# Kernel tuning notes

Hardware: AMD Instinct MI355X
Metric: run time of the kernel (lower is better)

The kernel has to match this reference:

```python
import jax, jax.numpy as jnp
import numpy as np

B, N, MW, H, C, K = 64, 8192, 128, 8, 1024, 3
HD = C // H  # head width = 128


def setup_inputs() -> dict:
    key = jax.random.key(0)
    ks = jax.random.split(key, 16)
    s = 0.02
    return {
        "control_state": jax.random.normal(ks[0], (B, C), jnp.float32),
        "memory": jax.random.normal(ks[1], (B, N, MW), jnp.float32),
        "prev_weights": jax.nn.softmax(jax.random.normal(ks[2], (B, H, N), jnp.float32), axis=-1),
        "defaults": jax.nn.softmax(jax.random.normal(ks[3], (B, H, N), jnp.float32), axis=-1),
        "W_head": s * jax.random.normal(ks[4], (C, H * HD), jnp.float32),
        "b_head": jnp.zeros((H, HD), jnp.float32),
        "W_reset": s * jax.random.normal(ks[5], (H, HD, 1), jnp.float32),
        "b_reset": jnp.zeros((H, 1), jnp.float32),
        "W_key": s * jax.random.normal(ks[6], (H, HD, MW), jnp.float32),
        "b_key": jnp.zeros((H, MW), jnp.float32),
        "W_beta": s * jax.random.normal(ks[7], (H, HD, 1), jnp.float32),
        "b_beta": jnp.zeros((H, 1), jnp.float32),
        "W_gate": s * jax.random.normal(ks[8], (H, HD, 1), jnp.float32),
        "b_gate": jnp.zeros((H, 1), jnp.float32),
        "W_shift": s * jax.random.normal(ks[9], (H, HD, K), jnp.float32),
        "b_shift": jnp.zeros((H, K), jnp.float32),
        "W_gamma": s * jax.random.normal(ks[10], (H, HD, 1), jnp.float32),
        "b_gamma": jnp.zeros((H, 1), jnp.float32),
        "merge_w": jax.random.normal(ks[11], (H,), jnp.float32) * 0.3 + 1.0 / H,
    }


def reference(control_state, memory, prev_weights, defaults, W_head, b_head,
              W_reset, b_reset, W_key, b_key, W_beta, b_beta, W_gate, b_gate,
              W_shift, b_shift, W_gamma, b_gamma, merge_w):
    eps = 1e-8
    # head projection: [B,C] -> [B,H,HD]
    heads = (control_state @ W_head).reshape(-1, H, HD) + b_head
    # sigmoid reset gate: convex blend of prior weights with defaults
    reset_p = jax.nn.sigmoid(jnp.einsum('bhd,hdo->bho', heads, W_reset) + b_reset)  # [B,H,1]
    weights = prev_weights * (1.0 - reset_p) + defaults * reset_p
    # NTM addressing parameters (per-head linear maps)
    key_ = jnp.einsum('bhd,hdw->bhw', heads, W_key) + b_key          # [B,H,MW]
    beta = jax.nn.softplus(jnp.einsum('bhd,hdo->bho', heads, W_beta) + b_beta)   # [B,H,1]
    gate = jax.nn.sigmoid(jnp.einsum('bhd,hdo->bho', heads, W_gate) + b_gate)    # [B,H,1]
    shift = jax.nn.softmax(jnp.einsum('bhd,hdk->bhk', heads, W_shift) + b_shift, axis=-1)  # [B,H,K]
    gamma = 1.0 + jax.nn.softplus(jnp.einsum('bhd,hdo->bho', heads, W_gamma) + b_gamma)    # [B,H,1]
    # content addressing: sharpened cosine similarity softmax over memory slots
    sim = jnp.einsum('bhw,bnw->bhn', key_, memory)
    sim = sim / (jnp.linalg.norm(key_, axis=-1, keepdims=True)
                 * jnp.linalg.norm(memory, axis=-1)[:, None, :] + eps)
    content = jax.nn.softmax(beta * sim, axis=-1)                    # [B,H,N]
    # interpolate with (possibly reset) prior weights
    w_g = gate * content + (1.0 - gate) * weights
    # location addressing: circular convolution with shift kernel symmetric around 0
    w_s = sum(shift[..., j:j + 1] * jnp.roll(w_g, j - K // 2, axis=-1) for j in range(K))
    # sharpening
    w_pow = (w_s + eps) ** gamma
    new_w = w_pow / jnp.sum(w_pow, axis=-1, keepdims=True)           # [B,H,N]
    # read: per-head attention matmul against memory, then weighted head merge
    headed = jnp.einsum('bhn,bnw->bhw', new_w, memory)               # [B,H,MW]
    out = jnp.einsum('bhw,h->bw', headed, merge_w)                   # [B,MW]
    return out, new_w
```

## Files before the change

kernel.cpp:

```cpp
#include <hip/hip_runtime.h>
#include <hip/hip_bf16.h>
#include <math.h>

#define Bb 64
#define Nn 8192
#define MWw 128
#define Hh 8
#define Cc 1024
#define HDd 128
#define Kk 3

__device__ __forceinline__ float dot4(float4 a, float4 b) {
  return a.x*b.x + a.y*b.y + a.z*b.z + a.w*b.w;
}
__device__ __forceinline__ float sigmoidf_(float x) { return 1.0f / (1.0f + __expf(-x)); }
__device__ __forceinline__ float softplusf_(float x) {
  return fmaxf(x, 0.0f) + log1pf(__expf(-fabsf(x)));
}

__global__ __launch_bounds__(1024) void k_params(
    const float* __restrict__ cs, const float* __restrict__ W_head, const float* __restrict__ b_head,
    const float* __restrict__ W_reset, const float* __restrict__ b_reset,
    const float* __restrict__ W_key, const float* __restrict__ b_key,
    const float* __restrict__ W_beta, const float* __restrict__ b_beta,
    const float* __restrict__ W_gate, const float* __restrict__ b_gate,
    const float* __restrict__ W_shift, const float* __restrict__ b_shift,
    const float* __restrict__ W_gamma, const float* __restrict__ b_gamma,
    float* __restrict__ key_ws, float* __restrict__ params,
    float* __restrict__ zs, float* __restrict__ outp)
{
  int bh = blockIdx.x;
  int b = bh >> 3, h = bh & 7;
  int t = threadIdx.x;
  int d = t & 127, sl = t >> 7;
  __shared__ float red[8][128];
  __shared__ float head_s[128];
  __shared__ float key_s[128];
  __shared__ float wred[16];

  if (bh == 0) {
    zs[t] = 0.0f;
    #pragma unroll
    for (int j = 0; j < 8; ++j) outp[j * 1024 + t] = 0.0f;
  }

  const float* csb = cs + b * Cc + sl * 128;
  const float* w0 = W_head + (size_t)(sl * 128) * (Hh * HDd) + h * HDd + d;
  float acc = 0.0f;
  #pragma unroll 8
  for (int c = 0; c < 128; ++c) acc = fmaf(csb[c], w0[(size_t)c * (Hh * HDd)], acc);
  red[sl][d] = acc;
  __syncthreads();
  if (t < 128) {
    float s = b_head[h * HDd + t];
    #pragma unroll
    for (int j = 0; j < 8; ++j) s += red[j][t];
    head_s[t] = s;
  }
  __syncthreads();

  {
    const float* wk = W_key + (size_t)h * HDd * MWw + (sl * 16) * MWw + d;
    float ka = 0.0f;
    #pragma unroll
    for (int dd = 0; dd < 16; ++dd) ka = fmaf(head_s[sl * 16 + dd], wk[dd * MWw], ka);
    red[sl][d] = ka;
  }
  __syncthreads();
  if (t < 128) {
    float kv = b_key[h * MWw + t];
    #pragma unroll
    for (int j = 0; j < 8; ++j) kv += red[j][t];
    key_ws[bh * MWw + t] = kv;
    key_s[t] = kv;
  }
  __syncthreads();

  float hd = head_s[d];
  float v;
  switch (sl) {
    case 0: v = hd * W_reset[h * HDd + d]; break;
    case 1: v = hd * W_beta[h * HDd + d]; break;
    case 2: v = hd * W_gate[h * HDd + d]; break;
    case 3: v = hd * W_gamma[h * HDd + d]; break;
    case 4: v = hd * W_shift[(h * HDd + d) * Kk + 0]; break;
    case 5: v = hd * W_shift[(h * HDd + d) * Kk + 1]; break;
    case 6: v = hd * W_shift[(h * HDd + d) * Kk + 2]; break;
    default: v = key_s[d] * key_s[d]; break;
  }
  v += __shfl_xor(v, 1, 64);
  v += __shfl_xor(v, 2, 64);
  v += __shfl_xor(v, 4, 64);
  v += __shfl_xor(v, 8, 64);
  v += __shfl_xor(v, 16, 64);
  v += __shfl_xor(v, 32, 64);
  if ((t & 63) == 0) wred[t >> 6] = v;
  __syncthreads();
  if (t == 0) {
    float r0 = wred[0]  + wred[1];
    float r1 = wred[2]  + wred[3];
    float r2 = wred[4]  + wred[5];
    float r3 = wred[6]  + wred[7];
    float r4 = wred[8]  + wred[9];
    float r5 = wred[10] + wred[11];
    float r6 = wred[12] + wred[13];
    float r7 = wred[14] + wred[15];
    float reset = sigmoidf_(r0 + b_reset[h]);
    float beta  = softplusf_(r1 + b_beta[h]);
    float gate  = sigmoidf_(r2 + b_gate[h]);
    float gamma = 1.0f + softplusf_(r3 + b_gamma[h]);
    float a0 = r4 + b_shift[h * Kk + 0];
    float a1 = r5 + b_shift[h * Kk + 1];
    float a2 = r6 + b_shift[h * Kk + 2];
    float mx = fmaxf(a0, fmaxf(a1, a2));
    float e0 = __expf(a0 - mx), e1 = __expf(a1 - mx), e2 = __expf(a2 - mx);
    float inv = 1.0f / (e0 + e1 + e2);
    float* P = params + bh * 8;
    P[0] = reset; P[1] = beta; P[2] = gate; P[3] = gamma;
    P[4] = e0 * inv; P[5] = e1 * inv; P[6] = e2 * inv;
    P[7] = sqrtf(r7);
  }
}

__global__ __launch_bounds__(256, 2) void k_sim(
    const float* __restrict__ mem, const float* __restrict__ key_ws,
    const float* __restrict__ params, float* __restrict__ e_ws, float* __restrict__ Z)
{
  int b = blockIdx.y, chunk = blockIdx.x;
  int t = threadIdx.x;
  int lane = t & 63, wid = t >> 6;
  int sub = lane & 7, rid = lane >> 3;
  __shared__ float4 keys[8][32];
  __shared__ float betas[8], knorms[8];
  __shared__ float e_s[8][520];
  if (t < 8) { betas[t] = params[(b * 8 + t) * 8 + 1]; knorms[t] = params[(b * 8 + t) * 8 + 7]; }
  {
    int h = t >> 5, q = t & 31;
    keys[h][q] = ((const float4*)key_ws)[(b * 8 + h) * 32 + q];
  }
  __syncthreads();

  float4 kreg[8][4];
  #pragma unroll
  for (int h2 = 0; h2 < 8; ++h2) {
    kreg[h2][0] = keys[h2][sub];
    kreg[h2][1] = keys[h2][sub + 8];
    kreg[h2][2] = keys[h2][sub + 16];
    kreg[h2][3] = keys[h2][sub + 24];
  }

  const float4* m4 = (const float4*)mem + (size_t)b * Nn * 32;
  float beta = betas[sub], kn = knorms[sub];
  float zloc = 0.0f;
  int n0 = chunk * 512;

  #pragma unroll 1
  for (int itr = 0; itr < 8; ++itr) {
    int nb = n0 + itr * 64 + wid * 16 + rid;
    float4 m[2][4];
    float nrm[2];
    float acc[2][8];
    #pragma unroll
    for (int r = 0; r < 2; ++r) {
      const float4* rp = m4 + (size_t)(nb + r * 8) * 32 + sub;
      m[r][0] = rp[0]; m[r][1] = rp[8]; m[r][2] = rp[16]; m[r][3] = rp[24];
    }
    #pragma unroll
    for (int r = 0; r < 2; ++r) {
      nrm[r] = dot4(m[r][0], m[r][0]) + dot4(m[r][1], m[r][1])
             + dot4(m[r][2], m[r][2]) + dot4(m[r][3], m[r][3]);
      #pragma unroll
      for (int h2 = 0; h2 < 8; ++h2) {
        acc[r][h2] = dot4(m[r][0], kreg[h2][0]) + dot4(m[r][1], kreg[h2][1])
                   + dot4(m[r][2], kreg[h2][2]) + dot4(m[r][3], kreg[h2][3]);
      }
    }
    #pragma unroll
    for (int r = 0; r < 2; ++r) {
      float* a = acc[r];
      bool h1 = (sub & 1) != 0;
      float v40 = (h1 ? a[1] : a[0]) + __shfl_xor(h1 ? a[0] : a[1], 1, 64);
      float v41 = (h1 ? a[3] : a[2]) + __shfl_xor(h1 ? a[2] : a[3], 1, 64);
      float v42 = (h1 ? a[5] : a[4]) + __shfl_xor(h1 ? a[4] : a[5], 1, 64);
      float v43 = (h1 ? a[7] : a[6]) + __shfl_xor(h1 ? a[6] : a[7], 1, 64);
      bool h2b = (sub & 2) != 0;
      float v20 = (h2b ? v41 : v40) + __shfl_xor(h2b ? v40 : v41, 2, 64);
      float v21 = (h2b ? v43 : v42) + __shfl_xor(h2b ? v42 : v43, 2, 64);
      bool h4 = (sub & 4) != 0;
      float dsum = (h4 ? v21 : v20) + __shfl_xor(h4 ? v20 : v21, 4, 64);
      float nr = nrm[r];
      nr += __shfl_xor(nr, 1, 64);
      nr += __shfl_xor(nr, 2, 64);
      nr += __shfl_xor(nr, 4, 64);
      float s = beta * dsum / (kn * sqrtf(nr) + 1e-8f);
      float e = __expf(s - beta);
      e_s[sub][(nb + r * 8) - n0] = e;
      zloc += e;
    }
  }
  zloc += __shfl_xor(zloc, 8, 64);
  zloc += __shfl_xor(zloc, 16, 64);
  zloc += __shfl_xor(zloc, 32, 64);
  if (lane < 8) atomicAdd(&Z[b * 8 + lane], zloc);
  __syncthreads();

  #pragma unroll
  for (int j = 0; j < 4; ++j) {
    int idx = j * 256 + t;
    int h = idx >> 7, q = idx & 127;
    float4 v = *(const float4*)&e_s[h][q * 4];
    ((float4*)(e_ws + (size_t)(b * 8 + h) * Nn + n0))[q] = v;
  }
}

__global__ __launch_bounds__(256) void k_conv(
    const float* __restrict__ e_ws, const float* __restrict__ prev, const float* __restrict__ defw,
    const float* __restrict__ params, const float* __restrict__ Z,
    float* __restrict__ wp, float* __restrict__ S)
{
  int chunk = blockIdx.x, h = blockIdx.y, b = blockIdx.z;
  int bh = b * 8 + h, t = threadIdx.x;
  __shared__ float wg[2052];
  const float* P = params + bh * 8;
  float reset = P[0], gate = P[2], gamma = P[3], s0 = P[4], s1 = P[5], s2 = P[6];
  float invZg = gate / Z[bh];
  float om = 1.0f - gate, omr = 1.0f - reset;
  size_t base = (size_t)bh * Nn;
  int n0 = chunk * 2048;

  const float4* e4p = (const float4*)(e_ws + base + n0);
  const float4* p4p = (const float4*)(prev + base + n0);
  const float4* d4p = (const float4*)(defw + base + n0);
  #pragma unroll
  for (int it = 0; it < 2; ++it) {
    int idx4 = it * 256 + t;
    float4 e = e4p[idx4], pv = p4p[idx4], dv = d4p[idx4];
    float4 w;
    w.x = invZg * e.x + om * (pv.x * omr + dv.x * reset);
    w.y = invZg * e.y + om * (pv.y * omr + dv.y * reset);
    w.z = invZg * e.z + om * (pv.z * omr + dv.z * reset);
    w.w = invZg * e.w + om * (pv.w * omr + dv.w * reset);
    *(float4*)&wg[idx4 * 4] = w;
  }
  if (t < 2) {
    int n = (t == 0) ? ((n0 + Nn - 1) & (Nn - 1)) : ((n0 + 2048) & (Nn - 1));
    float e = e_ws[base + n], pv = prev[base + n], dv = defw[base + n];
    wg[2048 + t] = invZg * e + om * (pv * omr + dv * reset);
  }
  __syncthreads();

  float sacc = 0.0f;
  float4* wp4 = (float4*)(wp + base + n0);
  #pragma unroll
  for (int it = 0; it < 2; ++it) {
    int idx4 = it * 256 + t;
    int l = idx4 * 4;
    float4 c = *(const float4*)&wg[l];
    float left  = (l == 0)        ? wg[2048] : wg[l - 1];
    float right = (l + 4 == 2048) ? wg[2049] : wg[l + 4];
    float4 wsv;
    wsv.x = s0 * c.y   + s1 * c.x + s2 * left;
    wsv.y = s0 * c.z   + s1 * c.y + s2 * c.x;
    wsv.z = s0 * c.w   + s1 * c.z + s2 * c.y;
    wsv.w = s0 * right + s1 * c.w + s2 * c.z;
    float4 o;
    o.x = __expf(gamma * __logf(wsv.x + 1e-8f));
    o.y = __expf(gamma * __logf(wsv.y + 1e-8f));
    o.z = __expf(gamma * __logf(wsv.z + 1e-8f));
    o.w = __expf(gamma * __logf(wsv.w + 1e-8f));
    wp4[idx4] = o;
    sacc += o.x + o.y + o.z + o.w;
  }
  sacc += __shfl_xor(sacc, 1, 64);
  sacc += __shfl_xor(sacc, 2, 64);
  sacc += __shfl_xor(sacc, 4, 64);
  sacc += __shfl_xor(sacc, 8, 64);
  sacc += __shfl_xor(sacc, 16, 64);
  sacc += __shfl_xor(sacc, 32, 64);
  __shared__ float sred[4];
  if ((t & 63) == 0) sred[t >> 6] = sacc;
  __syncthreads();
  if (t == 0) atomicAdd(&S[bh], sred[0] + sred[1] + sred[2] + sred[3]);
}

__global__ __launch_bounds__(256) void k_readnorm(
    const float* __restrict__ mem, float* __restrict__ wp, const float* __restrict__ S,
    const float* __restrict__ merge_w, float* __restrict__ out)
{
  int b = blockIdx.y; int n0 = blockIdx.x * 512; int t = threadIdx.x;
  __shared__ float kh[8], invS_s[8];
  __shared__ float coef_s[512];
  __shared__ float4 red4[256];
  if (t < 8) {
    float s = S[b * 8 + t];
    invS_s[t] = 1.0f / s;
    kh[t] = merge_w[t] / s;
  }
  __syncthreads();

  int col = t & 127, grp = t >> 7;
  float4 cf = make_float4(0.0f, 0.0f, 0.0f, 0.0f);
  #pragma unroll
  for (int hh = 0; hh < 4; ++hh) {
    int h = grp * 4 + hh;
    float4* wph = (float4*)(wp + (size_t)(b * 8 + h) * Nn + n0);
    float4 v = wph[col];
    float is = invS_s[h], k = kh[h];
    float4 o;
    o.x = v.x * is; o.y = v.y * is; o.z = v.z * is; o.w = v.w * is;
    wph[col] = o;
    cf.x = fmaf(k, v.x, cf.x);
    cf.y = fmaf(k, v.y, cf.y);
    cf.z = fmaf(k, v.z, cf.z);
    cf.w = fmaf(k, v.w, cf.w);
  }
  red4[grp * 128 + col] = cf;
  __syncthreads();
  if (t < 128) {
    float4 a = red4[t], c = red4[128 + t];
    float4 s4;
    s4.x = a.x + c.x; s4.y = a.y + c.y; s4.z = a.z + c.z; s4.w = a.w + c.w;
    *(float4*)&coef_s[t * 4] = s4;
  }
  __syncthreads();

  int w4 = t & 31, rg = t >> 5;
  const float4* m4 = (const float4*)mem + (size_t)b * Nn * 32;
  float4 acc = make_float4(0.0f, 0.0f, 0.0f, 0.0f);
  #pragma unroll 4
  for (int it = 0; it < 64; ++it) {
    int nl = it * 8 + rg;
    float c = coef_s[nl];
    float4 m = m4[(size_t)(n0 + nl) * 32 + w4];
    acc.x = fmaf(c, m.x, acc.x);
    acc.y = fmaf(c, m.y, acc.y);
    acc.z = fmaf(c, m.z, acc.z);
    acc.w = fmaf(c, m.w, acc.w);
  }
  red4[t] = acc;
  __syncthreads();
  if (t < 32) {
    float4 s = red4[t];
    #pragma unroll
    for (int j = 1; j < 8; ++j) {
      float4 o = red4[t + 32 * j];
      s.x += o.x; s.y += o.y; s.z += o.z; s.w += o.w;
    }
    atomicAdd(&out[b * MWw + t * 4 + 0], s.x);
    atomicAdd(&out[b * MWw + t * 4 + 1], s.y);
    atomicAdd(&out[b * MWw + t * 4 + 2], s.z);
    atomicAdd(&out[b * MWw + t * 4 + 3], s.w);
  }
}

extern "C" void kernel_launch(void* const* d_in, const int* in_sizes, int n_in,
                              void* d_out, int out_size, void* d_ws, size_t ws_size,
                              hipStream_t stream)
{
  const float* cs      = (const float*)d_in[0];
  const float* mem     = (const float*)d_in[1];
  const float* prev    = (const float*)d_in[2];
  const float* defw    = (const float*)d_in[3];
  const float* W_head  = (const float*)d_in[4];
  const float* b_head  = (const float*)d_in[5];
  const float* W_reset = (const float*)d_in[6];
  const float* b_reset = (const float*)d_in[7];
  const float* W_key   = (const float*)d_in[8];
  const float* b_key   = (const float*)d_in[9];
  const float* W_beta  = (const float*)d_in[10];
  const float* b_beta  = (const float*)d_in[11];
  const float* W_gate  = (const float*)d_in[12];
  const float* b_gate  = (const float*)d_in[13];
  const float* W_shift = (const float*)d_in[14];
  const float* b_shift = (const float*)d_in[15];
  const float* W_gamma = (const float*)d_in[16];
  const float* b_gamma = (const float*)d_in[17];
  const float* merge_w = (const float*)d_in[18];

  float* out  = (float*)d_out;
  float* neww = out + Bb * MWw;

  float* ws_f   = (float*)d_ws;
  float* key_ws = ws_f;
  float* params = ws_f + 65536;
  float* Zacc   = ws_f + 69632;
  float* Sacc   = ws_f + 70144;
  float* e_ws   = ws_f + 70656;

  k_params<<<dim3(Bb * Hh), dim3(1024), 0, stream>>>(
      cs, W_head, b_head, W_reset, b_reset, W_key, b_key, W_beta, b_beta,
      W_gate, b_gate, W_shift, b_shift, W_gamma, b_gamma, key_ws, params,
      Zacc, out);
  k_sim<<<dim3(16, Bb), dim3(256), 0, stream>>>(mem, key_ws, params, e_ws, Zacc);
  k_conv<<<dim3(4, Hh, Bb), dim3(256), 0, stream>>>(e_ws, prev, defw, params, Zacc, neww, Sacc);
  k_readnorm<<<dim3(16, Bb), dim3(256), 0, stream>>>(mem, neww, Sacc, merge_w, out);
}
```

Measured before the change: 495.1 us.

## Fuse similarity, convolution and read stages into one grid-synchronised kernel

```diff
diff --git a/kernel.cpp b/kernel.cpp
--- a/kernel.cpp
+++ b/kernel.cpp
@@ -1,5 +1,4 @@
 #include <hip/hip_runtime.h>
-#include <hip/hip_bf16.h>
 #include <math.h>
 
 #define Bb 64
@@ -16,6 +15,21 @@
 __device__ __forceinline__ float sigmoidf_(float x) { return 1.0f / (1.0f + __expf(-x)); }
 __device__ __forceinline__ float softplusf_(float x) {
   return fmaxf(x, 0.0f) + log1pf(__expf(-fabsf(x)));
+}
+
+__device__ __forceinline__ void grid_barrier(unsigned* bar, unsigned target) {
+  __syncthreads();
+  if (threadIdx.x == 0) {
+    __threadfence();
+    __hip_atomic_fetch_add(bar, 1u, __ATOMIC_ACQ_REL, __HIP_MEMORY_SCOPE_AGENT);
+    int spins = 0;
+    while (__hip_atomic_load(bar, __ATOMIC_ACQUIRE, __HIP_MEMORY_SCOPE_AGENT) < target) {
+      __builtin_amdgcn_s_sleep(8);
+      if (++spins > (1 << 22)) break;
+    }
+    __threadfence();
+  }
+  __syncthreads();
 }
 
 __global__ __launch_bounds__(1024) void k_params(
@@ -40,6 +54,7 @@
 
   if (bh == 0) {
     zs[t] = 0.0f;
+    if (t < 16) zs[1024 + t] = 0.0f;
     #pragma unroll
     for (int j = 0; j < 8; ++j) outp[j * 1024 + t] = 0.0f;
   }
@@ -122,22 +137,34 @@
   }
 }
 
-__global__ __launch_bounds__(256, 2) void k_sim(
+#define ESTRIDE 1032
+
+__global__ __launch_bounds__(256, 2) void k_fused(
     const float* __restrict__ mem, const float* __restrict__ key_ws,
-    const float* __restrict__ params, float* __restrict__ e_ws, float* __restrict__ Z)
+    const float* __restrict__ params, const float* __restrict__ prev,
+    const float* __restrict__ defw, const float* __restrict__ merge_w,
+    float* __restrict__ Z, float* __restrict__ S, float* __restrict__ eh,
+    unsigned* __restrict__ bar, float* __restrict__ neww, float* __restrict__ out)
 {
-  int b = blockIdx.y, chunk = blockIdx.x;
+  int c = blockIdx.x, b = blockIdx.y;
   int t = threadIdx.x;
   int lane = t & 63, wid = t >> 6;
   int sub = lane & 7, rid = lane >> 3;
+  int n0 = c * 1024;
+
   __shared__ float4 keys[8][32];
   __shared__ float betas[8], knorms[8];
-  __shared__ float e_s[8][520];
+  __shared__ float e_s[8 * ESTRIDE];
+  __shared__ float pL[64];
+  __shared__ float zL[8];
+  __shared__ float wgh[2][8];
+  __shared__ float kh_s[8], invS_s[8];
+  __shared__ float coef_s[1024];
+  __shared__ float4 red4[256];
+
   if (t < 8) { betas[t] = params[(b * 8 + t) * 8 + 1]; knorms[t] = params[(b * 8 + t) * 8 + 7]; }
-  {
-    int h = t >> 5, q = t & 31;
-    keys[h][q] = ((const float4*)key_ws)[(b * 8 + h) * 32 + q];
-  }
+  { int h = t >> 5, q = t & 31;
+    keys[h][q] = ((const float4*)key_ws)[(b * 8 + h) * 32 + q]; }
   __syncthreads();
 
   float4 kreg[8][4];
@@ -152,17 +179,16 @@
   const float4* m4 = (const float4*)mem + (size_t)b * Nn * 32;
   float beta = betas[sub], kn = knorms[sub];
   float zloc = 0.0f;
-  int n0 = chunk * 512;
 
   #pragma unroll 1
-  for (int itr = 0; itr < 8; ++itr) {
-    int nb = n0 + itr * 64 + wid * 16 + rid;
+  for (int itr = 0; itr < 16; ++itr) {
+    int nl = itr * 64 + wid * 16 + rid;
     float4 m[2][4];
     float nrm[2];
     float acc[2][8];
     #pragma unroll
     for (int r = 0; r < 2; ++r) {
-      const float4* rp = m4 + (size_t)(nb + r * 8) * 32 + sub;
+      const float4* rp = m4 + (size_t)(n0 + nl + r * 8) * 32 + sub;
       m[r][0] = rp[0]; m[r][1] = rp[8]; m[r][2] = rp[16]; m[r][3] = rp[24];
     }
     #pragma unroll
@@ -194,7 +220,7 @@
       nr += __shfl_xor(nr, 4, 64);
       float s = beta * dsum / (kn * sqrtf(nr) + 1e-8f);
       float e = __expf(s - beta);
-      e_s[sub][(nb + r * 8) - n0] = e;
+      e_s[sub * ESTRIDE + nl + r * 8] = e;
       zloc += e;
     }
   }
@@ -203,148 +229,137 @@
   zloc += __shfl_xor(zloc, 32, 64);
   if (lane < 8) atomicAdd(&Z[b * 8 + lane], zloc);
   __syncthreads();
+  if (t < 16) {
+    int hh = t & 7, side = t >> 3;
+    __hip_atomic_store(&eh[(b * 8 + c) * 16 + side * 8 + hh],
+                       e_s[hh * ESTRIDE + (side ? 1023 : 0)],
+                       __ATOMIC_RELAXED, __HIP_MEMORY_SCOPE_AGENT);
+  }
+  grid_barrier(&bar[0], 512u);
+
+  if (t < 64) pL[t] = params[b * 64 + t];
+  if (t < 8)
+    zL[t] = __hip_atomic_load(&Z[b * 8 + t], __ATOMIC_RELAXED, __HIP_MEMORY_SCOPE_AGENT);
+  __syncthreads();
+
+  int h = t >> 5, q = t & 31;
+  float reset = pL[h * 8 + 0], gate = pL[h * 8 + 2], gamma = pL[h * 8 + 3];
+  float s0 = pL[h * 8 + 4], s1 = pL[h * 8 + 5], s2 = pL[h * 8 + 6];
+  float invZg = gate / zL[h];
+  float om = 1.0f - gate, omr = 1.0f - reset;
+  size_t gbase = (size_t)(b * 8 + h) * Nn + n0;
+  const float4* p4 = (const float4*)(prev + gbase);
+  const float4* d4 = (const float4*)(defw + gbase);
+  float* wgp = &e_s[h * ESTRIDE];
 
   #pragma unroll
-  for (int j = 0; j < 4; ++j) {
-    int idx = j * 256 + t;
-    int h = idx >> 7, q = idx & 127;
-    float4 v = *(const float4*)&e_s[h][q * 4];
-    ((float4*)(e_ws + (size_t)(b * 8 + h) * Nn + n0))[q] = v;
-  }
-}
-
-__global__ __launch_bounds__(256) void k_conv(
-    const float* __restrict__ e_ws, const float* __restrict__ prev, const float* __restrict__ defw,
-    const float* __restrict__ params, const float* __restrict__ Z,
-    float* __restrict__ wp, float* __restrict__ S)
-{
-  int chunk = blockIdx.x, h = blockIdx.y, b = blockIdx.z;
-  int bh = b * 8 + h, t = threadIdx.x;
-  __shared__ float wg[2052];
-  const float* P = params + bh * 8;
-  float reset = P[0], gate = P[2], gamma = P[3], s0 = P[4], s1 = P[5], s2 = P[6];
-  float invZg = gate / Z[bh];
-  float om = 1.0f - gate, omr = 1.0f - reset;
-  size_t base = (size_t)bh * Nn;
-  int n0 = chunk * 2048;
-
-  const float4* e4p = (const float4*)(e_ws + base + n0);
-  const float4* p4p = (const float4*)(prev + base + n0);
-  const float4* d4p = (const float4*)(defw + base + n0);
+  for (int k = 0; k < 8; ++k) {
+    int q4 = q + 32 * k;
+    float4 e4 = *(const float4*)&wgp[q4 * 4];
+    float4 pv = p4[q4], dv = d4[q4];
+    float4 w;
+    w.x = invZg * e4.x + om * (pv.x * omr + dv.x * reset);
+    w.y = invZg * e4.y + om * (pv.y * omr + dv.y * reset);
+    w.z = invZg * e4.z + om * (pv.z * omr + dv.z * reset);
+    w.w = invZg * e4.w + om * (pv.w * omr + dv.w * reset);
+    *(float4*)&wgp[q4 * 4] = w;
+  }
+  if (t < 16) {
+    int hh = t & 7, side = t >> 3;
+    int nbr = side ? ((c + 1) & 7) : ((c + 7) & 7);
+    float e = __hip_atomic_load(&eh[(b * 8 + nbr) * 16 + (side ? 0 : 8) + hh],
+                                __ATOMIC_RELAXED, __HIP_MEMORY_SCOPE_AGENT);
+    int hrow = side ? ((n0 + 1024) & (Nn - 1)) : ((n0 + Nn - 1) & (Nn - 1));
+    float rst = pL[hh * 8 + 0], gt = pL[hh * 8 + 2];
+    float iZg = gt / zL[hh];
+    size_t gi = (size_t)(b * 8 + hh) * Nn + hrow;
+    wgh[side][hh] = iZg * e + (1.0f - gt) * (prev[gi] * (1.0f - rst) + defw[gi] * rst);
+  }
+  __syncthreads();
+
+  float4 o[8];
+  float sacc = 0.0f;
   #pragma unroll
-  for (int it = 0; it < 2; ++it) {
-    int idx4 = it * 256 + t;
-    float4 e = e4p[idx4], pv = p4p[idx4], dv = d4p[idx4];
-    float4 w;
-    w.x = invZg * e.x + om * (pv.x * omr + dv.x * reset);
-    w.y = invZg * e.y + om * (pv.y * omr + dv.y * reset);
-    w.z = invZg * e.z + om * (pv.z * omr + dv.z * reset);
-    w.w = invZg * e.w + om * (pv.w * omr + dv.w * reset);
-    *(float4*)&wg[idx4 * 4] = w;
-  }
-  if (t < 2) {
-    int n = (t == 0) ? ((n0 + Nn - 1) & (Nn - 1)) : ((n0 + 2048) & (Nn - 1));
-    float e = e_ws[base + n], pv = prev[base + n], dv = defw[base + n];
-    wg[2048 + t] = invZg * e + om * (pv * omr + dv * reset);
-  }
-  __syncthreads();
-
-  float sacc = 0.0f;
-  float4* wp4 = (float4*)(wp + base + n0);
+  for (int k = 0; k < 8; ++k) {
+    int q4 = q + 32 * k;
+    int l = q4 * 4;
+    float4 c4 = *(const float4*)&wgp[l];
+    float left  = (l == 0)        ? wgh[0][h] : wgp[l - 1];
+    float right = (l + 4 == 1024) ? wgh[1][h] : wgp[l + 4];
+    float4 wsv;
+    wsv.x = s0 * c4.y   + s1 * c4.x + s2 * left;
+    wsv.y = s0 * c4.z   + s1 * c4.y + s2 * c4.x;
+    wsv.z = s0 * c4.w   + s1 * c4.z + s2 * c4.y;
+    wsv.w = s0 * right  + s1 * c4.w + s2 * c4.z;
+    o[k].x = __expf(gamma * __logf(wsv.x + 1e-8f));
+    o[k].y = __expf(gamma * __logf(wsv.y + 1e-8f));
+    o[k].z = __expf(gamma * __logf(wsv.z + 1e-8f));
+    o[k].w = __expf(gamma * __logf(wsv.w + 1e-8f));
+    sacc += o[k].x + o[k].y + o[k].z + o[k].w;
+  }
+  __syncthreads();
   #pragma unroll
-  for (int it = 0; it < 2; ++it) {
-    int idx4 = it * 256 + t;
-    int l = idx4 * 4;
-    float4 c = *(const float4*)&wg[l];
-    float left  = (l == 0)        ? wg[2048] : wg[l - 1];
-    float right = (l + 4 == 2048) ? wg[2049] : wg[l + 4];
-    float4 wsv;
-    wsv.x = s0 * c.y   + s1 * c.x + s2 * left;
-    wsv.y = s0 * c.z   + s1 * c.y + s2 * c.x;
-    wsv.z = s0 * c.w   + s1 * c.z + s2 * c.y;
-    wsv.w = s0 * right + s1 * c.w + s2 * c.z;
-    float4 o;
-    o.x = __expf(gamma * __logf(wsv.x + 1e-8f));
-    o.y = __expf(gamma * __logf(wsv.y + 1e-8f));
-    o.z = __expf(gamma * __logf(wsv.z + 1e-8f));
-    o.w = __expf(gamma * __logf(wsv.w + 1e-8f));
-    wp4[idx4] = o;
-    sacc += o.x + o.y + o.z + o.w;
-  }
+  for (int k = 0; k < 8; ++k) *(float4*)&wgp[(q + 32 * k) * 4] = o[k];
   sacc += __shfl_xor(sacc, 1, 64);
   sacc += __shfl_xor(sacc, 2, 64);
   sacc += __shfl_xor(sacc, 4, 64);
   sacc += __shfl_xor(sacc, 8, 64);
   sacc += __shfl_xor(sacc, 16, 64);
-  sacc += __shfl_xor(sacc, 32, 64);
-  __shared__ float sred[4];
-  if ((t & 63) == 0) sred[t >> 6] = sacc;
-  __syncthreads();
-  if (t == 0) atomicAdd(&S[bh], sred[0] + sred[1] + sred[2] + sred[3]);
-}
-
-__global__ __launch_bounds__(256) void k_readnorm(
-    const float* __restrict__ mem, float* __restrict__ wp, const float* __restrict__ S,
-    const float* __restrict__ merge_w, float* __restrict__ out)
-{
-  int b = blockIdx.y; int n0 = blockIdx.x * 512; int t = threadIdx.x;
-  __shared__ float kh[8], invS_s[8];
-  __shared__ float coef_s[512];
-  __shared__ float4 red4[256];
+  if ((t & 31) == 0) atomicAdd(&S[b * 8 + h], sacc);
+  grid_barrier(&bar[1], 512u);
+
   if (t < 8) {
-    float s = S[b * 8 + t];
+    float s = __hip_atomic_load(&S[b * 8 + t], __ATOMIC_RELAXED, __HIP_MEMORY_SCOPE_AGENT);
     invS_s[t] = 1.0f / s;
-    kh[t] = merge_w[t] / s;
-  }
-  __syncthreads();
-
-  int col = t & 127, grp = t >> 7;
-  float4 cf = make_float4(0.0f, 0.0f, 0.0f, 0.0f);
+    kh_s[t] = merge_w[t] / s;
+  }
+  __syncthreads();
+
+  float invS = invS_s[h];
+  float4* nw4 = (float4*)(neww + gbase);
   #pragma unroll
-  for (int hh = 0; hh < 4; ++hh) {
-    int h = grp * 4 + hh;
-    float4* wph = (float4*)(wp + (size_t)(b * 8 + h) * Nn + n0);
-    float4 v = wph[col];
-    float is = invS_s[h], k = kh[h];
-    float4 o;
-    o.x = v.x * is; o.y = v.y * is; o.z = v.z * is; o.w = v.w * is;
-    wph[col] = o;
-    cf.x = fmaf(k, v.x, cf.x);
-    cf.y = fmaf(k, v.y, cf.y);
-    cf.z = fmaf(k, v.z, cf.z);
-    cf.w = fmaf(k, v.w, cf.w);
-  }
-  red4[grp * 128 + col] = cf;
-  __syncthreads();
-  if (t < 128) {
-    float4 a = red4[t], c = red4[128 + t];
-    float4 s4;
-    s4.x = a.x + c.x; s4.y = a.y + c.y; s4.z = a.z + c.z; s4.w = a.w + c.w;
-    *(float4*)&coef_s[t * 4] = s4;
+  for (int k = 0; k < 8; ++k) {
+    int q4 = q + 32 * k;
+    float4 v = *(const float4*)&wgp[q4 * 4];
+    float4 on;
+    on.x = v.x * invS; on.y = v.y * invS; on.z = v.z * invS; on.w = v.w * invS;
+    nw4[q4] = on;
+  }
+  {
+    float4 cf = make_float4(0.0f, 0.0f, 0.0f, 0.0f);
+    #pragma unroll
+    for (int hh = 0; hh < 8; ++hh) {
+      float4 v = *(const float4*)&e_s[hh * ESTRIDE + t * 4];
+      float k = kh_s[hh];
+      cf.x = fmaf(k, v.x, cf.x);
+      cf.y = fmaf(k, v.y, cf.y);
+      cf.z = fmaf(k, v.z, cf.z);
+      cf.w = fmaf(k, v.w, cf.w);
+    }
+    *(float4*)&coef_s[t * 4] = cf;
   }
   __syncthreads();
 
   int w4 = t & 31, rg = t >> 5;
-  const float4* m4 = (const float4*)mem + (size_t)b * Nn * 32;
-  float4 acc = make_float4(0.0f, 0.0f, 0.0f, 0.0f);
+  float4 acc2 = make_float4(0.0f, 0.0f, 0.0f, 0.0f);
   #pragma unroll 4
-  for (int it = 0; it < 64; ++it) {
+  for (int it = 0; it < 128; ++it) {
     int nl = it * 8 + rg;
-    float c = coef_s[nl];
-    float4 m = m4[(size_t)(n0 + nl) * 32 + w4];
-    acc.x = fmaf(c, m.x, acc.x);
-    acc.y = fmaf(c, m.y, acc.y);
-    acc.z = fmaf(c, m.z, acc.z);
-    acc.w = fmaf(c, m.w, acc.w);
-  }
-  red4[t] = acc;
+    float cf = coef_s[nl];
+    float4 mv = m4[(size_t)(n0 + nl) * 32 + w4];
+    acc2.x = fmaf(cf, mv.x, acc2.x);
+    acc2.y = fmaf(cf, mv.y, acc2.y);
+    acc2.z = fmaf(cf, mv.z, acc2.z);
+    acc2.w = fmaf(cf, mv.w, acc2.w);
+  }
+  red4[t] = acc2;
   __syncthreads();
   if (t < 32) {
     float4 s = red4[t];
     #pragma unroll
     for (int j = 1; j < 8; ++j) {
-      float4 o = red4[t + 32 * j];
-      s.x += o.x; s.y += o.y; s.z += o.z; s.w += o.w;
+      float4 ov = red4[t + 32 * j];
+      s.x += ov.x; s.y += ov.y; s.z += ov.z; s.w += ov.w;
     }
     atomicAdd(&out[b * MWw + t * 4 + 0], s.x);
     atomicAdd(&out[b * MWw + t * 4 + 1], s.y);
@@ -385,13 +400,15 @@
   float* params = ws_f + 65536;
   float* Zacc   = ws_f + 69632;
   float* Sacc   = ws_f + 70144;
-  float* e_ws   = ws_f + 70656;
+  unsigned* bar = (unsigned*)(ws_f + 70656);
+  float* ehalo  = ws_f + 70672;
 
   k_params<<<dim3(Bb * Hh), dim3(1024), 0, stream>>>(
       cs, W_head, b_head, W_reset, b_reset, W_key, b_key, W_beta, b_beta,
       W_gate, b_gate, W_shift, b_shift, W_gamma, b_gamma, key_ws, params,
       Zacc, out);
-  k_sim<<<dim3(16, Bb), dim3(256), 0, stream>>>(mem, key_ws, params, e_ws, Zacc);
-  k_conv<<<dim3(4, Hh, Bb), dim3(256), 0, stream>>>(e_ws, prev, defw, params, Zacc, neww, Sacc);
-  k_readnorm<<<dim3(16, Bb), dim3(256), 0, stream>>>(mem, neww, Sacc, merge_w, out);
-}
+
+  k_fused<<<dim3(8, Bb), dim3(256), 0, stream>>>(
+      mem, key_ws, params, prev, defw, merge_w, Zacc, Sacc, ehalo, bar,
+      neww, out);
+}
```

After: 594.0 us. 1.2x slower.
